# Optimization experiments

Hardware: AMD Instinct MI355X
Metric: run time of the kernel (lower is better)

Reference implementation:

```python
import jax, jax.numpy as jnp
import numpy as np

B, N, ENC, DEC, E, ATT, V, T = 64, 196, 2048, 512, 512, 512, 32000, 32


def setup_inputs() -> dict:
    key = jax.random.key(0)
    ks = jax.random.split(key, 12)
    s = 0.02  # param init scale
    f = lambda k, shape: jax.random.normal(k, shape, jnp.float32) * s
    return {
        "features": jax.random.normal(ks[0], (B, N, ENC), jnp.float32),
        "captions": jax.random.randint(ks[1], (B, T), 0, V),
        "emb": f(ks[2], (V, E)),
        "att_Wenc": f(ks[3], (ENC, ATT)),
        "att_Wdec": f(ks[4], (DEC, ATT)),
        "att_v": f(ks[5], (ATT,)),
        "init_h_W": f(ks[6], (ENC, DEC)), "init_h_b": jnp.zeros((DEC,), jnp.float32),
        "init_c_W": f(ks[7], (ENC, DEC)), "init_c_b": jnp.zeros((DEC,), jnp.float32),
        "W_ih": f(ks[8], (4 * DEC, E + ENC)), "W_hh": f(ks[9], (4 * DEC, DEC)),
        "b_ih": jnp.zeros((4 * DEC,), jnp.float32), "b_hh": jnp.zeros((4 * DEC,), jnp.float32),
        "out_W": f(ks[10], (DEC, V)), "out_b": jnp.zeros((V,), jnp.float32),
    }


def reference(features, captions, emb, att_Wenc, att_Wdec, att_v,
              init_h_W, init_h_b, init_c_W, init_c_b,
              W_ih, W_hh, b_ih, b_hh, out_W, out_b):
    # init hidden/cell from mean-pooled encoder features
    mean_f = features.mean(axis=1)                      # [B, ENC]
    h = mean_f @ init_h_W + init_h_b                    # [B, DEC]
    c = mean_f @ init_c_W + init_c_b                    # [B, DEC]

    enc_att = features @ att_Wenc                       # [B, N, ATT] (loop-invariant)
    embs = emb[captions]                                # [B, T, E]
    xs = jnp.swapaxes(embs[:, :-1], 0, 1)               # [T-1, B, E] time-major

    def step(carry, x):
        h, c = carry
        # Bahdanau attention: tanh(Wf + Wh) . v -> softmax over spatial locations
        e = jnp.tanh(enc_att + (h @ att_Wdec)[:, None, :]) @ att_v   # [B, N]
        alpha = jax.nn.softmax(e, axis=1)                            # [B, N]
        context = jnp.einsum('bn,bnd->bd', alpha, features)          # [B, ENC]
        lstm_in = jnp.concatenate([x, context], axis=1)              # [B, E+ENC]
        gates = lstm_in @ W_ih.T + b_ih + h @ W_hh.T + b_hh          # [B, 4*DEC]
        i, f, g, o = jnp.split(gates, 4, axis=1)                     # torch gate order
        c = jax.nn.sigmoid(f) * c + jax.nn.sigmoid(i) * jnp.tanh(g)
        h = jax.nn.sigmoid(o) * jnp.tanh(c)
        out = h @ out_W + out_b                                      # dropout = identity (eval)
        return (h, c), (out, alpha)

    _, (preds, alphas) = jax.lax.scan(step, (h, c), xs)
    # back to batch-major: preds [B, T-1, V], alphas [B, T-1, N]
    return jnp.swapaxes(preds, 0, 1), jnp.swapaxes(alphas, 0, 1)
```

## Files before the change

kernel.cpp:

```cpp
#include <hip/hip_runtime.h>
#include <math.h>

constexpr int kB = 64, kN = 196, kENC = 2048, kDEC = 512, kE = 512, kATT = 512;
constexpr int kV = 32000, kT = 32, kTS = 31;
constexpr int kKIH = kE + kENC;
constexpr int kKG  = kENC + kDEC;
constexpr int kG   = 4 * kDEC;
constexpr int kSPL = 8, kKSP = kKG / kSPL;
constexpr int kM   = kTS * kB;
constexpr int kMP  = 2048;

typedef __attribute__((ext_vector_type(8))) short bf8;
typedef __attribute__((ext_vector_type(4))) float f4;
typedef __attribute__((ext_vector_type(4))) unsigned u4;

__device__ __forceinline__ f4 mfma16(bf8 a, bf8 b, f4 c){
  asm("v_mfma_f32_16x16x32_bf16 %0, %1, %2, %0" : "+v"(c) : "v"(a), "v"(b));
  return c;
}
__device__ __forceinline__ float bf2f(unsigned short u){
  return __uint_as_float(((unsigned)u) << 16);
}
__device__ __forceinline__ unsigned short f2b(float f){
  unsigned u = __float_as_uint(f);
  u += 0x7fffu + ((u >> 16) & 1u);
  return (unsigned short)(u >> 16);
}
__device__ __forceinline__ float th_(float x){
  float e2 = __expf(2.f * x);
  return 1.f - 2.f * __builtin_amdgcn_rcpf(e2 + 1.f);
}
__device__ __forceinline__ float sg_(float x){
  return __builtin_amdgcn_rcpf(1.f + __expf(-x));
}

__global__ void k_cvt(const float* __restrict__ src, unsigned short* __restrict__ dst, int n8){
  int i = blockIdx.x * 256 + threadIdx.x;
  if (i >= n8) return;
  float4 a = ((const float4*)src)[2 * i];
  float4 b = ((const float4*)src)[2 * i + 1];
  union { unsigned short u[8]; uint4 v; } t;
  t.u[0] = f2b(a.x); t.u[1] = f2b(a.y); t.u[2] = f2b(a.z); t.u[3] = f2b(a.w);
  t.u[4] = f2b(b.x); t.u[5] = f2b(b.y); t.u[6] = f2b(b.z); t.u[7] = f2b(b.w);
  ((uint4*)dst)[i] = t.v;
}

__global__ __launch_bounds__(256) void k_cvtmean(const float* __restrict__ feat,
        unsigned short* __restrict__ featb, float* __restrict__ meanp){
  int b = blockIdx.x, nq = blockIdx.y, tid = threadIdx.x;
  int d0 = tid * 8;
  const float* fp = feat + (size_t)b * kN * kENC + d0;
  unsigned short* op = featb + (size_t)b * kN * kENC + d0;
  float s[8] = {0.f,0.f,0.f,0.f,0.f,0.f,0.f,0.f};
  int nbeg = nq * 49, nend = nbeg + 49;
  #pragma unroll 4
  for (int n = nbeg; n < nend; ++n){
    float4 a = *(const float4*)(fp + (size_t)n * kENC);
    float4 c = *(const float4*)(fp + (size_t)n * kENC + 4);
    union { unsigned short u[8]; u4 v; } t;
    t.u[0] = f2b(a.x); t.u[1] = f2b(a.y); t.u[2] = f2b(a.z); t.u[3] = f2b(a.w);
    t.u[4] = f2b(c.x); t.u[5] = f2b(c.y); t.u[6] = f2b(c.z); t.u[7] = f2b(c.w);
    *(u4*)(op + (size_t)n * kENC) = t.v;
    s[0] += a.x; s[1] += a.y; s[2] += a.z; s[3] += a.w;
    s[4] += c.x; s[5] += c.y; s[6] += c.z; s[7] += c.w;
  }
  float* mp = meanp + ((size_t)b * 4 + nq) * kENC + d0;
  #pragma unroll
  for (int j = 0; j < 8; j++) mp[j] = s[j];
}

__global__ __launch_bounds__(256) void k_tcvt(const float* __restrict__ src,
                                              unsigned short* __restrict__ dst, int R, int C){
  __shared__ float t[32][33];
  int c0 = blockIdx.x * 32, r0 = blockIdx.y * 32;
  int tx = threadIdx.x & 31, ty = threadIdx.x >> 5;
  #pragma unroll
  for (int j = 0; j < 4; j++)
    t[ty + 8*j][tx] = src[(size_t)(r0 + ty + 8*j) * C + c0 + tx];
  __syncthreads();
  #pragma unroll
  for (int j = 0; j < 4; j++)
    dst[(size_t)(c0 + ty + 8*j) * R + r0 + tx] = f2b(t[tx][ty + 8*j]);
}

__global__ __launch_bounds__(256) void k_tf32(const float* __restrict__ src,
                                              float* __restrict__ dst, int R, int C){
  __shared__ float t[32][33];
  int c0 = blockIdx.x * 32, r0 = blockIdx.y * 32;
  int tx = threadIdx.x & 31, ty = threadIdx.x >> 5;
  #pragma unroll
  for (int j = 0; j < 4; j++)
    t[ty + 8*j][tx] = src[(size_t)(r0 + ty + 8*j) * C + c0 + tx];
  __syncthreads();
  #pragma unroll
  for (int j = 0; j < 4; j++)
    dst[(size_t)(c0 + ty + 8*j) * R + r0 + tx] = t[tx][ty + 8*j];
}

__global__ __launch_bounds__(512) void k_init(const float* __restrict__ meanp,
                       const float* __restrict__ Wh, const float* __restrict__ bh,
                       const float* __restrict__ Wc, const float* __restrict__ bc,
                       float* __restrict__ h, float* __restrict__ c){
  __shared__ float mf[kENC];
  int b = blockIdx.x;
  const float* mp = meanp + (size_t)b * 4 * kENC;
  for (int i = threadIdx.x; i < kENC; i += 512)
    mf[i] = (mp[i] + mp[kENC + i] + mp[2*kENC + i] + mp[3*kENC + i]) * (1.f / kN);
  __syncthreads();
  int j = threadIdx.x;
  const float* W  = blockIdx.y ? Wc : Wh;
  const float* bb = blockIdx.y ? bc : bh;
  float acc = bb[j];
  for (int k = 0; k < kENC; k++) acc = fmaf(mf[k], W[k * kDEC + j], acc);
  (blockIdx.y ? c : h)[b * kDEC + j] = acc;
}

__global__ __launch_bounds__(512) void k_gather(const float* __restrict__ emb,
        const int* __restrict__ captions, unsigned short* __restrict__ Xemb){
  int m = blockIdx.x;
  int t = m >> 6, b = m & 63, d = threadIdx.x;
  Xemb[(size_t)m * kE + d] = f2b(emb[(size_t)captions[b * kT + t] * kE + d]);
}

template<int K, int LDA, int LDB, int LDC>
__global__ __launch_bounds__(256) void k_gemm_nt(const unsigned short* __restrict__ A,
                                                 const unsigned short* __restrict__ Bt,
                                                 unsigned short* __restrict__ Cb){
  int w = threadIdx.x >> 6, lane = threadIdx.x & 63;
  int m0 = blockIdx.x * 64 + w * 16, n0 = blockIdx.y * 64;
  int lr = lane & 15, lk = (lane >> 4) * 8;
  f4 acc[4] = {};
  const unsigned short* Ap = A  + (size_t)(m0 + lr) * LDA + lk;
  const unsigned short* Bp = Bt + (size_t)(n0 + lr) * LDB + lk;
  #pragma unroll 4
  for (int k0 = 0; k0 < K; k0 += 32){
    bf8 a  = *(const bf8*)(Ap + k0);
    bf8 b0 = *(const bf8*)(Bp + k0);
    bf8 b1 = *(const bf8*)(Bp + (size_t)16 * LDB + k0);
    bf8 b2 = *(const bf8*)(Bp + (size_t)32 * LDB + k0);
    bf8 b3 = *(const bf8*)(Bp + (size_t)48 * LDB + k0);
    acc[0] = mfma16(a, b0, acc[0]); acc[1] = mfma16(a, b1, acc[1]);
    acc[2] = mfma16(a, b2, acc[2]); acc[3] = mfma16(a, b3, acc[3]);
  }
  asm volatile("s_nop 7\n\ts_nop 7");
  int orow = (lane >> 4) * 4;
  #pragma unroll
  for (int nt = 0; nt < 4; nt++)
    #pragma unroll
    for (int r = 0; r < 4; r++)
      Cb[(size_t)(m0 + orow + r) * LDC + n0 + nt*16 + lr] = f2b(acc[nt][r]);
}

__global__ __launch_bounds__(256) void k_e(const unsigned short* __restrict__ EA,
                   const float* __restrict__ hWdec,
                   const float* __restrict__ attv, float* __restrict__ e){
  int w = threadIdx.x >> 6, lane = threadIdx.x & 63;
  int r = blockIdx.x * 4 + w;
  int b = r / kN;
  u4 ev = *(const u4*)(EA + (size_t)r * kATT + lane * 8);
  const float* hp = hWdec + b * kATT + lane * 8;
  const float* ap = attv + lane * 8;
  float4 h0 = *(const float4*)hp, h1 = *(const float4*)(hp + 4);
  float4 v0 = *(const float4*)ap, v1 = *(const float4*)(ap + 4);
  float s = 0.f;
  s = fmaf(th_(bf2f((unsigned short)(ev.x & 0xffffu)) + h0.x), v0.x, s);
  s = fmaf(th_(bf2f((unsigned short)(ev.x >> 16))     + h0.y), v0.y, s);
  s = fmaf(th_(bf2f((unsigned short)(ev.y & 0xffffu)) + h0.z), v0.z, s);
  s = fmaf(th_(bf2f((unsigned short)(ev.y >> 16))     + h0.w), v0.w, s);
  s = fmaf(th_(bf2f((unsigned short)(ev.z & 0xffffu)) + h1.x), v1.x, s);
  s = fmaf(th_(bf2f((unsigned short)(ev.z >> 16))     + h1.y), v1.y, s);
  s = fmaf(th_(bf2f((unsigned short)(ev.w & 0xffffu)) + h1.z), v1.z, s);
  s = fmaf(th_(bf2f((unsigned short)(ev.w >> 16))     + h1.w), v1.w, s);
  #pragma unroll
  for (int off = 32; off; off >>= 1) s += __shfl_xor(s, off, 64);
  if (lane == 0) e[r] = s;
}

__global__ __launch_bounds__(256) void k_ctx(const float* __restrict__ e,
                     const unsigned short* __restrict__ featb,
                     unsigned short* __restrict__ Xb, float* __restrict__ alphas, int t){
  __shared__ float al[kN];
  __shared__ float red[256];
  __shared__ float cred[4][64][8];
  int b = blockIdx.x, q = blockIdx.y, tid = threadIdx.x;
  float ev = (tid < kN) ? e[b * kN + tid] : -1e30f;
  red[tid] = ev; __syncthreads();
  for (int off = 128; off; off >>= 1){ if (tid < off) red[tid] = fmaxf(red[tid], red[tid + off]); __syncthreads(); }
  float mx = red[0]; __syncthreads();
  float ex = (tid < kN) ? __expf(ev - mx) : 0.f;
  red[tid] = ex; __syncthreads();
  for (int off = 128; off; off >>= 1){ if (tid < off) red[tid] += red[tid + off]; __syncthreads(); }
  float inv = 1.f / red[0];
  if (tid < kN){
    float a = ex * inv;
    al[tid] = a;
    if (q == 0) alphas[((size_t)b * kTS + t) * kN + tid] = a;
  }
  __syncthreads();
  int g = tid & 63, nq = tid >> 6;
  int d0 = q * 512 + g * 8;
  const unsigned short* fp = featb + (size_t)b * kN * kENC + d0;
  float c[8] = {0.f,0.f,0.f,0.f,0.f,0.f,0.f,0.f};
  int nbeg = nq * 49, nend = nbeg + 49;
  #pragma unroll 7
  for (int n = nbeg; n < nend; ++n){
    u4 v = *(const u4*)(fp + (size_t)n * kENC);
    float a = al[n];
    c[0] = fmaf(bf2f((unsigned short)(v.x & 0xffffu)), a, c[0]);
    c[1] = fmaf(bf2f((unsigned short)(v.x >> 16)),     a, c[1]);
    c[2] = fmaf(bf2f((unsigned short)(v.y & 0xffffu)), a, c[2]);
    c[3] = fmaf(bf2f((unsigned short)(v.y >> 16)),     a, c[3]);
    c[4] = fmaf(bf2f((unsigned short)(v.z & 0xffffu)), a, c[4]);
    c[5] = fmaf(bf2f((unsigned short)(v.z >> 16)),     a, c[5]);
    c[6] = fmaf(bf2f((unsigned short)(v.w & 0xffffu)), a, c[6]);
    c[7] = fmaf(bf2f((unsigned short)(v.w >> 16)),     a, c[7]);
  }
  if (nq){
    #pragma unroll
    for (int j = 0; j < 8; j++) cred[nq][g][j] = c[j];
  }
  __syncthreads();
  if (nq == 0){
    unsigned outw[4];
    #pragma unroll
    for (int j = 0; j < 4; j++){
      float lo = c[2*j]   + cred[1][g][2*j]   + cred[2][g][2*j]   + cred[3][g][2*j];
      float hi = c[2*j+1] + cred[1][g][2*j+1] + cred[2][g][2*j+1] + cred[3][g][2*j+1];
      outw[j] = ((unsigned)f2b(hi) << 16) | (unsigned)f2b(lo);
    }
    *(u4*)(Xb + (size_t)b * kKG + d0) = *(u4*)outw;
  }
}

__global__ __launch_bounds__(256) void k_gates(const unsigned short* __restrict__ X,
        const unsigned short* __restrict__ Wih, const unsigned short* __restrict__ Whh,
        float* __restrict__ gpart){
  int w = threadIdx.x >> 6, lane = threadIdx.x & 63;
  int n0 = blockIdx.x * 64 + w * 16, ks = blockIdx.y;
  int lr = lane & 15, lk = (lane >> 4) * 8;
  int nrow = n0 + lr;
  f4 acc[4] = {};
  const unsigned short* Xp = X + (size_t)lr * kKG + ks * kKSP + lk;
  #pragma unroll 2
  for (int kt = 0; kt < kKSP; kt += 32){
    int kk = ks * kKSP + kt + lk;
    bf8 a0 = *(const bf8*)(Xp + kt);
    bf8 a1 = *(const bf8*)(Xp + 16 * kKG + kt);
    bf8 a2 = *(const bf8*)(Xp + 32 * kKG + kt);
    bf8 a3 = *(const bf8*)(Xp + 48 * kKG + kt);
    const unsigned short* bp = (kk < kENC) ? (Wih + (size_t)nrow * kKIH + kE + kk)
                                           : (Whh + (size_t)nrow * kDEC + (kk - kENC));
    bf8 b = *(const bf8*)bp;
    acc[0] = mfma16(a0, b, acc[0]); acc[1] = mfma16(a1, b, acc[1]);
    acc[2] = mfma16(a2, b, acc[2]); acc[3] = mfma16(a3, b, acc[3]);
  }
  asm volatile("s_nop 7\n\ts_nop 7");
  float* gp = gpart + (size_t)ks * kB * kG;
  int orow = (lane >> 4) * 4;
  #pragma unroll
  for (int mt = 0; mt < 4; mt++)
    #pragma unroll
    for (int r = 0; r < 4; r++)
      gp[(size_t)(mt*16 + orow + r) * kG + n0 + lr] = acc[mt][r];
}

__global__ __launch_bounds__(512) void k_lstm(const float* __restrict__ gpart,
      const unsigned short* __restrict__ Gxb,
      const float* __restrict__ bih, const float* __restrict__ bhh,
      float* __restrict__ c, unsigned short* __restrict__ Xb,
      unsigned short* __restrict__ Hall,
      const float* __restrict__ WdecT, float* __restrict__ hWdec, int t){
  __shared__ float hl[kDEC];
  int b = blockIdx.x, d = threadIdx.x;
  int m = t * kB + b;
  float gi = 0.f, gf = 0.f, gg = 0.f, go = 0.f;
  for (int ks = 0; ks < kSPL; ks++){
    const float* gp = gpart + ((size_t)ks * kB + b) * kG;
    gi += gp[d]; gf += gp[kDEC + d]; gg += gp[2*kDEC + d]; go += gp[3*kDEC + d];
  }
  const unsigned short* gx = Gxb + (size_t)m * kG;
  gi += bf2f(gx[d])          + bih[d]          + bhh[d];
  gf += bf2f(gx[kDEC + d])   + bih[kDEC + d]   + bhh[kDEC + d];
  gg += bf2f(gx[2*kDEC + d]) + bih[2*kDEC + d] + bhh[2*kDEC + d];
  go += bf2f(gx[3*kDEC + d]) + bih[3*kDEC + d] + bhh[3*kDEC + d];
  float cn = sg_(gf) * c[b*kDEC + d] + sg_(gi) * th_(gg);
  float hn = sg_(go) * th_(cn);
  c[b*kDEC + d] = cn;
  hl[d] = hn;
  unsigned short hb = f2b(hn);
  Xb[(size_t)b*kKG + kENC + d] = hb;
  Hall[((size_t)b*kTS + t)*kDEC + d] = hb;
  __syncthreads();
  const float* wr = WdecT + (size_t)d * kATT;
  float a = 0.f;
  #pragma unroll 8
  for (int kk = 0; kk < kATT; kk += 4){
    float4 wv = *(const float4*)(wr + kk);
    a = fmaf(wv.x, hl[kk + 0], a);
    a = fmaf(wv.y, hl[kk + 1], a);
    a = fmaf(wv.z, hl[kk + 2], a);
    a = fmaf(wv.w, hl[kk + 3], a);
  }
  hWdec[b * kATT + d] = a;
}

__global__ __launch_bounds__(512) void k_prep(const float* __restrict__ h0,
      unsigned short* __restrict__ Xb,
      const float* __restrict__ WdecT, float* __restrict__ hWdec){
  __shared__ float hl[kDEC];
  int b = blockIdx.x, d = threadIdx.x;
  float hv = h0[b*kDEC + d];
  hl[d] = hv;
  Xb[(size_t)b*kKG + kENC + d] = f2b(hv);
  __syncthreads();
  const float* wr = WdecT + (size_t)d * kATT;
  float a = 0.f;
  #pragma unroll 8
  for (int kk = 0; kk < kATT; kk += 4){
    float4 wv = *(const float4*)(wr + kk);
    a = fmaf(wv.x, hl[kk + 0], a);
    a = fmaf(wv.y, hl[kk + 1], a);
    a = fmaf(wv.z, hl[kk + 2], a);
    a = fmaf(wv.w, hl[kk + 3], a);
  }
  hWdec[b * kATT + d] = a;
}

constexpr int kLDW = 132;
__global__ __launch_bounds__(512) void k_bigout(const unsigned short* __restrict__ Hall,
        const unsigned short* __restrict__ Wt,
        const float* __restrict__ bias, float* __restrict__ preds){
  __shared__ float st[64][kLDW];
  int w = threadIdx.x >> 6, lane = threadIdx.x & 63;
  int m0 = blockIdx.x * 256;
  int n0 = blockIdx.y * 128;
  int lr = lane & 15, lk = (lane >> 4) * 8;
  f4 acc[2][8];
  #pragma unroll
  for (int nt = 0; nt < 8; nt++){
    float bv = bias[n0 + nt*16 + lr];
    acc[0][nt] = (f4){bv, bv, bv, bv};
    acc[1][nt] = (f4){bv, bv, bv, bv};
  }
  const unsigned short* Ap = Hall + (size_t)(m0 + w*32 + lr) * kDEC + lk;
  const unsigned short* Bp = Wt + (size_t)(n0 + lr) * kDEC + lk;
  #pragma unroll 2
  for (int k0 = 0; k0 < kDEC; k0 += 32){
    bf8 a0 = *(const bf8*)(Ap + k0);
    bf8 a1 = *(const bf8*)(Ap + 16*kDEC + k0);
    #pragma unroll
    for (int nt = 0; nt < 8; nt++){
      bf8 b = *(const bf8*)(Bp + (size_t)nt*16*kDEC + k0);
      acc[0][nt] = mfma16(a0, b, acc[0][nt]);
      acc[1][nt] = mfma16(a1, b, acc[1][nt]);
    }
  }
  asm volatile("s_nop 7\n\ts_nop 7");
  int orow = (lane >> 4) * 4;
  for (int c = 0; c < 4; c++){
    __syncthreads();
    if ((w >> 1) == c){
      int rbase = (w & 1) * 32;
      #pragma unroll
      for (int half = 0; half < 2; half++)
        #pragma unroll
        for (int nt = 0; nt < 8; nt++)
          #pragma unroll
          for (int r = 0; r < 4; r++)
            st[rbase + half*16 + orow + r][nt*16 + lr] = acc[half][nt][r];
    }
    __syncthreads();
    int mbase = m0 + c*64;
    #pragma unroll
    for (int p = 0; p < 4; p++){
      int idx = threadIdx.x + p*512;
      int row = idx >> 5, c4 = idx & 31;
      int m = mbase + row;
      if (m < kM){
        float4 v = *(const float4*)(&st[row][c4*4]);
        *(float4*)(preds + (size_t)m * kV + n0 + c4*4) = v;
      }
    }
  }
}

extern "C" void kernel_launch(void* const* d_in, const int* in_sizes, int n_in,
                              void* d_out, int out_size, void* d_ws, size_t ws_size,
                              hipStream_t stream) {
  const float* feat     = (const float*)d_in[0];
  const int*   captions = (const int*)  d_in[1];
  const float* emb      = (const float*)d_in[2];
  const float* attWenc  = (const float*)d_in[3];
  const float* attWdec  = (const float*)d_in[4];
  const float* attv     = (const float*)d_in[5];
  const float* ihW      = (const float*)d_in[6];
  const float* ihb      = (const float*)d_in[7];
  const float* icW      = (const float*)d_in[8];
  const float* icb      = (const float*)d_in[9];
  const float* Wih      = (const float*)d_in[10];
  const float* Whh      = (const float*)d_in[11];
  const float* bih      = (const float*)d_in[12];
  const float* bhh      = (const float*)d_in[13];
  const float* outW     = (const float*)d_in[14];
  const float* outb     = (const float*)d_in[15];

  float* preds  = (float*)d_out;
  float* alphas = preds + (size_t)kB * kTS * kV;

  char* p = (char*)d_ws;
  unsigned short* featb  = (unsigned short*)p; p += (size_t)kB*kN*kENC*2;
  unsigned short* outWb  = (unsigned short*)p; p += (size_t)kV*kDEC*2;
  unsigned short* Wihb   = (unsigned short*)p; p += (size_t)kG*kKIH*2;
  unsigned short* Whhb   = (unsigned short*)p; p += (size_t)kG*kDEC*2;
  unsigned short* attWT  = (unsigned short*)p; p += (size_t)kATT*kENC*2;
  unsigned short* encattb= (unsigned short*)p; p += (size_t)kB*kN*kATT*2;
  unsigned short* Gxb    = (unsigned short*)p; p += (size_t)kMP*kG*2;
  unsigned short* Hall   = (unsigned short*)p; p += (size_t)kMP*kDEC*2;
  unsigned short* Xemb   = Hall;
  unsigned short* Xb     = (unsigned short*)p; p += (size_t)kB*kKG*2;
  float* WdecTf = (float*)p; p += (size_t)kATT*kDEC*4;
  float* gpart  = (float*)p; p += (size_t)kSPL*kB*kG*4;
  float* meanp  = (float*)p; p += (size_t)kB*4*kENC*4;
  float* hbuf   = (float*)p; p += (size_t)kB*kDEC*4;
  float* cws    = (float*)p; p += (size_t)kB*kDEC*4;
  float* hWdec  = (float*)p; p += (size_t)kB*kATT*4;
  float* evec   = (float*)p; p += (size_t)kB*kN*4;

  k_cvtmean<<<dim3(kB, 4), 256, 0, stream>>>(feat, featb, meanp);
  k_cvt<<<(kG*kKIH/8 + 255)/256, 256, 0, stream>>>(Wih, Wihb, kG*kKIH/8);
  k_cvt<<<(kG*kDEC/8 + 255)/256, 256, 0, stream>>>(Whh, Whhb, kG*kDEC/8);
  k_tcvt<<<dim3(kATT/32, kENC/32), 256, 0, stream>>>(attWenc, attWT, kENC, kATT);
  k_tf32<<<dim3(kATT/32, kDEC/32), 256, 0, stream>>>(attWdec, WdecTf, kDEC, kATT);
  k_tcvt<<<dim3(kV/32, kDEC/32), 256, 0, stream>>>(outW, outWb, kDEC, kV);

  k_init<<<dim3(kB, 2), 512, 0, stream>>>(meanp, ihW, ihb, icW, icb, hbuf, cws);

  k_gather<<<kM, 512, 0, stream>>>(emb, captions, Xemb);
  k_gemm_nt<kE, kE, kKIH, kG><<<dim3(kMP/64, kG/64), 256, 0, stream>>>(Xemb, Wihb, Gxb);

  k_gemm_nt<kENC, kENC, kENC, kATT><<<dim3(kB*kN/64, kATT/64), 256, 0, stream>>>(featb, attWT, encattb);

  k_prep<<<kB, 512, 0, stream>>>(hbuf, Xb, WdecTf, hWdec);

  for (int t = 0; t < kTS; ++t) {
    k_e<<<kB*kN/4, 256, 0, stream>>>(encattb, hWdec, attv, evec);
    k_ctx<<<dim3(kB, 4), 256, 0, stream>>>(evec, featb, Xb, alphas, t);
    k_gates<<<dim3(kG/64, kSPL), 256, 0, stream>>>(Xb, Wihb, Whhb, gpart);
    k_lstm<<<kB, 512, 0, stream>>>(gpart, Gxb, bih, bhh, cws, Xb, Hall,
                                   WdecTf, hWdec, t);
  }

  k_bigout<<<dim3(kMP/256, kV/128), 512, 0, stream>>>(Hall, outWb, outb, preds);
}
```

Before: 2.506 ms.

## Fuse attention score computation into softmax-context kernel and reorder encatt GEMM grid

Merges the per-step attention energy kernel into the softmax/context kernel, so each (batch, quarter) block computes all 196 energies itself. This removes one launch per timestep and the round trip of the energy vector through global memory. The cost is that the energy work is done redundantly by the four q-blocks per batch, with only 4 waves each. The encoder-attention GEMM gets its own kernel with the grid transposed so blocks sharing an A tile run adjacently. The preds output now uses nontemporal stores.

Measured after the change: 3.233 ms. 29.0% more time.

```diff
diff --git a/kernel.cpp b/kernel.cpp
--- a/kernel.cpp
+++ b/kernel.cpp
@@ -151,46 +151,78 @@
       Cb[(size_t)(m0 + orow + r) * LDC + n0 + nt*16 + lr] = f2b(acc[nt][r]);
 }
 
-__global__ __launch_bounds__(256) void k_e(const unsigned short* __restrict__ EA,
-                   const float* __restrict__ hWdec,
-                   const float* __restrict__ attv, float* __restrict__ e){
+__global__ __launch_bounds__(256) void k_encatt_nf(const unsigned short* __restrict__ A,
+                                                   const unsigned short* __restrict__ Bt,
+                                                   unsigned short* __restrict__ Cb){
   int w = threadIdx.x >> 6, lane = threadIdx.x & 63;
-  int r = blockIdx.x * 4 + w;
-  int b = r / kN;
-  u4 ev = *(const u4*)(EA + (size_t)r * kATT + lane * 8);
-  const float* hp = hWdec + b * kATT + lane * 8;
-  const float* ap = attv + lane * 8;
-  float4 h0 = *(const float4*)hp, h1 = *(const float4*)(hp + 4);
-  float4 v0 = *(const float4*)ap, v1 = *(const float4*)(ap + 4);
-  float s = 0.f;
-  s = fmaf(th_(bf2f((unsigned short)(ev.x & 0xffffu)) + h0.x), v0.x, s);
-  s = fmaf(th_(bf2f((unsigned short)(ev.x >> 16))     + h0.y), v0.y, s);
-  s = fmaf(th_(bf2f((unsigned short)(ev.y & 0xffffu)) + h0.z), v0.z, s);
-  s = fmaf(th_(bf2f((unsigned short)(ev.y >> 16))     + h0.w), v0.w, s);
-  s = fmaf(th_(bf2f((unsigned short)(ev.z & 0xffffu)) + h1.x), v1.x, s);
-  s = fmaf(th_(bf2f((unsigned short)(ev.z >> 16))     + h1.y), v1.y, s);
-  s = fmaf(th_(bf2f((unsigned short)(ev.w & 0xffffu)) + h1.z), v1.z, s);
-  s = fmaf(th_(bf2f((unsigned short)(ev.w >> 16))     + h1.w), v1.w, s);
-  #pragma unroll
-  for (int off = 32; off; off >>= 1) s += __shfl_xor(s, off, 64);
-  if (lane == 0) e[r] = s;
-}
-
-__global__ __launch_bounds__(256) void k_ctx(const float* __restrict__ e,
+  int n0 = blockIdx.x * 64;
+  int m0 = blockIdx.y * 64 + w * 16;
+  int lr = lane & 15, lk = (lane >> 4) * 8;
+  f4 acc[4] = {};
+  const unsigned short* Ap = A  + (size_t)(m0 + lr) * kENC + lk;
+  const unsigned short* Bp = Bt + (size_t)(n0 + lr) * kENC + lk;
+  #pragma unroll 4
+  for (int k0 = 0; k0 < kENC; k0 += 32){
+    bf8 a  = *(const bf8*)(Ap + k0);
+    bf8 b0 = *(const bf8*)(Bp + k0);
+    bf8 b1 = *(const bf8*)(Bp + (size_t)16 * kENC + k0);
+    bf8 b2 = *(const bf8*)(Bp + (size_t)32 * kENC + k0);
+    bf8 b3 = *(const bf8*)(Bp + (size_t)48 * kENC + k0);
+    acc[0] = mfma16(a, b0, acc[0]); acc[1] = mfma16(a, b1, acc[1]);
+    acc[2] = mfma16(a, b2, acc[2]); acc[3] = mfma16(a, b3, acc[3]);
+  }
+  asm volatile("s_nop 7\n\ts_nop 7");
+  int orow = (lane >> 4) * 4;
+  #pragma unroll
+  for (int nt = 0; nt < 4; nt++)
+    #pragma unroll
+    for (int r = 0; r < 4; r++)
+      Cb[(size_t)(m0 + orow + r) * kATT + n0 + nt*16 + lr] = f2b(acc[nt][r]);
+}
+
+__global__ __launch_bounds__(256) void k_att(const unsigned short* __restrict__ EA,
+                     const float* __restrict__ hWdec, const float* __restrict__ attv,
                      const unsigned short* __restrict__ featb,
                      unsigned short* __restrict__ Xb, float* __restrict__ alphas, int t){
   __shared__ float al[kN];
   __shared__ float red[256];
   __shared__ float cred[4][64][8];
   int b = blockIdx.x, q = blockIdx.y, tid = threadIdx.x;
-  float ev = (tid < kN) ? e[b * kN + tid] : -1e30f;
-  red[tid] = ev; __syncthreads();
+  int w = tid >> 6, lane = tid & 63;
+  {
+    float hw[8], av[8];
+    const float* hp = hWdec + b * kATT + lane * 8;
+    const float* ap = attv + lane * 8;
+    #pragma unroll
+    for (int u = 0; u < 8; u++){ hw[u] = hp[u]; av[u] = ap[u]; }
+    const unsigned short* eb = EA + (size_t)b * kN * kATT;
+    int rbeg = w * 49, rend = rbeg + 49;
+    for (int r = rbeg; r < rend; ++r){
+      u4 ev = *(const u4*)(eb + (size_t)r * kATT + lane * 8);
+      float s = 0.f;
+      s = fmaf(th_(bf2f((unsigned short)(ev.x & 0xffffu)) + hw[0]), av[0], s);
+      s = fmaf(th_(bf2f((unsigned short)(ev.x >> 16))     + hw[1]), av[1], s);
+      s = fmaf(th_(bf2f((unsigned short)(ev.y & 0xffffu)) + hw[2]), av[2], s);
+      s = fmaf(th_(bf2f((unsigned short)(ev.y >> 16))     + hw[3]), av[3], s);
+      s = fmaf(th_(bf2f((unsigned short)(ev.z & 0xffffu)) + hw[4]), av[4], s);
+      s = fmaf(th_(bf2f((unsigned short)(ev.z >> 16))     + hw[5]), av[5], s);
+      s = fmaf(th_(bf2f((unsigned short)(ev.w & 0xffffu)) + hw[6]), av[6], s);
+      s = fmaf(th_(bf2f((unsigned short)(ev.w >> 16))     + hw[7]), av[7], s);
+      #pragma unroll
+      for (int off = 32; off; off >>= 1) s += __shfl_xor(s, off, 64);
+      if (lane == 0) al[r] = s;
+    }
+  }
+  __syncthreads();
+  float ev2 = (tid < kN) ? al[tid] : -1e30f;
+  red[tid] = ev2; __syncthreads();
   for (int off = 128; off; off >>= 1){ if (tid < off) red[tid] = fmaxf(red[tid], red[tid + off]); __syncthreads(); }
   float mx = red[0]; __syncthreads();
-  float ex = (tid < kN) ? __expf(ev - mx) : 0.f;
+  float ex = (tid < kN) ? __expf(ev2 - mx) : 0.f;
   red[tid] = ex; __syncthreads();
   for (int off = 128; off; off >>= 1){ if (tid < off) red[tid] += red[tid + off]; __syncthreads(); }
   float inv = 1.f / red[0];
+  __syncthreads();
   if (tid < kN){
     float a = ex * inv;
     al[tid] = a;
@@ -377,8 +409,8 @@
       int row = idx >> 5, c4 = idx & 31;
       int m = mbase + row;
       if (m < kM){
-        float4 v = *(const float4*)(&st[row][c4*4]);
-        *(float4*)(preds + (size_t)m * kV + n0 + c4*4) = v;
+        f4 v = *(const f4*)(&st[row][c4*4]);
+        __builtin_nontemporal_store(v, (f4*)(preds + (size_t)m * kV + n0 + c4*4));
       }
     }
   }
@@ -424,7 +456,6 @@
   float* hbuf   = (float*)p; p += (size_t)kB*kDEC*4;
   float* cws    = (float*)p; p += (size_t)kB*kDEC*4;
   float* hWdec  = (float*)p; p += (size_t)kB*kATT*4;
-  float* evec   = (float*)p; p += (size_t)kB*kN*4;
 
   k_cvtmean<<<dim3(kB, 4), 256, 0, stream>>>(feat, featb, meanp);
   k_cvt<<<(kG*kKIH/8 + 255)/256, 256, 0, stream>>>(Wih, Wihb, kG*kKIH/8);
@@ -438,13 +469,12 @@
   k_gather<<<kM, 512, 0, stream>>>(emb, captions, Xemb);
   k_gemm_nt<kE, kE, kKIH, kG><<<dim3(kMP/64, kG/64), 256, 0, stream>>>(Xemb, Wihb, Gxb);
 
-  k_gemm_nt<kENC, kENC, kENC, kATT><<<dim3(kB*kN/64, kATT/64), 256, 0, stream>>>(featb, attWT, encattb);
+  k_encatt_nf<<<dim3(kATT/64, kB*kN/64), 256, 0, stream>>>(featb, attWT, encattb);
 
   k_prep<<<kB, 512, 0, stream>>>(hbuf, Xb, WdecTf, hWdec);
 
   for (int t = 0; t < kTS; ++t) {
-    k_e<<<kB*kN/4, 256, 0, stream>>>(encattb, hWdec, attv, evec);
-    k_ctx<<<dim3(kB, 4), 256, 0, stream>>>(evec, featb, Xb, alphas, t);
+    k_att<<<dim3(kB, 4), 256, 0, stream>>>(encattb, hWdec, attv, featb, Xb, alphas, t);
     k_gates<<<dim3(kG/64, kSPL), 256, 0, stream>>>(Xb, Wihb, Whhb, gpart);
     k_lstm<<<kB, 512, 0, stream>>>(gpart, Gxb, bih, bhh, cws, Xb, Hall,
                                    WdecTf, hWdec, t);
```
